# Kernel tuning notes

Hardware: AMD Instinct MI355X
Metric: run time of the kernel (lower is better)

## Reference

```python
import jax, jax.numpy as jnp
import numpy as np

CONTEXT_SIZE = 32
NDIM = 64
HEAD_SIZE = 64
BATCH = 16384


def setup_inputs() -> dict:
    key = jax.random.key(0)
    kx, kk, kq, kv = jax.random.split(key, 4)
    x = jax.random.normal(kx, (BATCH, CONTEXT_SIZE, NDIM), dtype=jnp.float32)
    # nn.Linear(ndim, head_size, bias=False): y = x @ W.T, W is [head_size, ndim].
    # We store transposed weights [ndim, head_size] so y = x @ W.
    scale = 1.0 / np.sqrt(NDIM)
    Wk = jax.random.normal(kk, (NDIM, HEAD_SIZE), dtype=jnp.float32) * scale
    Wq = jax.random.normal(kq, (NDIM, HEAD_SIZE), dtype=jnp.float32) * scale
    Wv = jax.random.normal(kv, (NDIM, HEAD_SIZE), dtype=jnp.float32) * scale
    return {"x": x, "Wk": Wk, "Wq": Wq, "Wv": Wv}


def reference(x, Wk, Wq, Wv):
    # x: [B, T, D] with T == CONTEXT_SIZE
    k = x @ Wk  # [B, T, H]
    q = x @ Wq  # [B, T, H]
    v = x @ Wv  # [B, T, H]
    # Faithful to source: p = q @ k^T / head_size**(-0.5) == q @ k^T * sqrt(head_size)
    p = jnp.einsum("bth,bsh->bts", q, k) * jnp.sqrt(jnp.float32(HEAD_SIZE))
    causal = jnp.tril(jnp.ones((CONTEXT_SIZE, CONTEXT_SIZE), dtype=bool))
    p = jnp.where(causal, p, -jnp.inf)
    p = jax.nn.softmax(p, axis=-1)
    # dropout is identity in eval mode
    return jnp.einsum("bts,bsh->bth", p, v)  # [B, T, H]
```

## Files before the change

kernel.cpp:

```cpp
#include <hip/hip_runtime.h>

typedef __attribute__((ext_vector_type(8))) short short8;
typedef __attribute__((ext_vector_type(4))) float f32x4;
typedef __attribute__((ext_vector_type(2))) unsigned int u32x2;

#define CTX 32
#define ND  64
#define NH  64
#define LOG2E_8 11.541560327111707f
#define NB_PER_WAVE 2

#define OFF_MH 0
#define OFF_ML 8192
#define OFF_WAVE 16384
#define PWSTR 80
#define PW_RTH 0
#define PW_RTL 2560
#define PW_VT  0
#define PW_P   4096
#define WAVE_BYTES 6144
#define LDS_BYTES (OFF_WAVE + 4 * WAVE_BYTES)

__device__ __forceinline__ unsigned short f2bf(float f) {
  unsigned int u = __builtin_bit_cast(unsigned int, f);
  u += 0x7FFFu + ((u >> 16) & 1u);
  return (unsigned short)(u >> 16);
}
__device__ __forceinline__ float bf2f(unsigned short b) {
  unsigned int u = ((unsigned int)b) << 16;
  return __builtin_bit_cast(float, u);
}
__device__ __forceinline__ unsigned int pk2(float a, float b) {
  return (unsigned int)f2bf(a) | ((unsigned int)f2bf(b) << 16);
}

#define MFMA(a, b, c) __builtin_amdgcn_mfma_f32_16x16x32_bf16((a), (b), (c), 0, 0, 0)

__global__ __launch_bounds__(256) void mk_m(
    const float* __restrict__ Wq, const float* __restrict__ Wk,
    const float* __restrict__ Wv,
    unsigned short* __restrict__ MtH, unsigned short* __restrict__ MtL,
    unsigned short* __restrict__ WvT)
{
  const int idx = blockIdx.x * 256 + threadIdx.x;
  const int dp = idx >> 6, d = idx & 63;
  const float* wq = Wq + d * 64;
  const float* wk = Wk + dp * 64;
  float acc = 0.f;
  #pragma unroll
  for (int h = 0; h < 64; ++h) acc = fmaf(wq[h], wk[h], acc);
  acc *= LOG2E_8;
  const unsigned short hi = f2bf(acc);
  MtH[idx] = hi;
  MtL[idx] = f2bf(acc - bf2f(hi));
  WvT[idx] = f2bf(Wv[d * 64 + dp]);
}

__device__ __forceinline__ void load_x(const float* __restrict__ xb,
                                       f32x4 (&xr)[2][2][2], int c, int g) {
  #pragma unroll
  for (int mt = 0; mt < 2; ++mt)
    #pragma unroll
    for (int kt = 0; kt < 2; ++kt) {
      const float* p = xb + (16 * mt + c) * ND + 32 * kt + 8 * g;
      xr[mt][kt][0] = *(const f32x4*)(p);
      xr[mt][kt][1] = *(const f32x4*)(p + 4);
    }
}

__device__ __forceinline__ void compute_batch(
    const f32x4 (&xr)[2][2][2], const short8 (&bvr)[4][2], char* lds, char* wl,
    float* __restrict__ ob, int c, int g)
{
  short8 xh[2][2], xl[2][2];
  #pragma unroll
  for (int mt = 0; mt < 2; ++mt) {
    #pragma unroll
    for (int kt = 0; kt < 2; ++kt) {
      short8 hi, lo;
      #pragma unroll
      for (int half = 0; half < 2; ++half) {
        #pragma unroll
        for (int j = 0; j < 4; ++j) {
          const float f = xr[mt][kt][half][j];
          const unsigned short h = f2bf(f);
          hi[4 * half + j] = (short)h;
          lo[4 * half + j] = (short)f2bf(f - bf2f(h));
        }
      }
      xh[mt][kt] = hi;
      xl[mt][kt] = lo;
    }
  }

  f32x4 pa[2][2] = {{{0.f,0.f,0.f,0.f},{0.f,0.f,0.f,0.f}},
                    {{0.f,0.f,0.f,0.f},{0.f,0.f,0.f,0.f}}};
  #pragma unroll
  for (int kt = 0; kt < 2; ++kt) {
    #pragma unroll
    for (int ntl = 0; ntl < 2; ++ntl) {
      const int nt = 2 * kt + ntl;
      f32x4 a0 = {0.f, 0.f, 0.f, 0.f};
      f32x4 a1 = {0.f, 0.f, 0.f, 0.f};
      #pragma unroll
      for (int kk = 0; kk < 2; ++kk) {
        const int row = 16 * nt + c;
        const int byte = row * 128 + ((64 * kk + 16 * g) ^ ((row & 7) << 4));
        const short8 bh = *(const short8*)(lds + OFF_MH + byte);
        const short8 bl = *(const short8*)(lds + OFF_ML + byte);
        a0 = MFMA(xh[0][kk], bh, a0);
        a0 = MFMA(xh[0][kk], bl, a0);
        a0 = MFMA(xl[0][kk], bh, a0);
        a1 = MFMA(xh[1][kk], bh, a1);
        a1 = MFMA(xh[1][kk], bl, a1);
        a1 = MFMA(xl[1][kk], bh, a1);
      }
      #pragma unroll
      for (int j = 0; j < 4; ++j) {
        const int col2 = 2 * (16 * ntl + c);
        const int off0 = (4 * g + j) * PWSTR + col2;
        const int off1 = (16 + 4 * g + j) * PWSTR + col2;
        const unsigned short h0 = f2bf(a0[j]);
        *(unsigned short*)(wl + PW_RTH + off0) = h0;
        *(unsigned short*)(wl + PW_RTL + off0) = f2bf(a0[j] - bf2f(h0));
        const unsigned short h1 = f2bf(a1[j]);
        *(unsigned short*)(wl + PW_RTH + off1) = h1;
        *(unsigned short*)(wl + PW_RTL + off1) = f2bf(a1[j] - bf2f(h1));
      }
    }
    short8 tH[2], tL[2];
    #pragma unroll
    for (int i = 0; i < 2; ++i) {
      const int off = (16 * i + c) * PWSTR + 16 * g;
      tH[i] = *(const short8*)(wl + PW_RTH + off);
      tL[i] = *(const short8*)(wl + PW_RTL + off);
    }
    #pragma unroll
    for (int mt = 0; mt < 2; ++mt) {
      #pragma unroll
      for (int nt2 = 0; nt2 < 2; ++nt2) {
        pa[mt][nt2] = MFMA(xh[mt][kt], tH[nt2], pa[mt][nt2]);
        pa[mt][nt2] = MFMA(xl[mt][kt], tH[nt2], pa[mt][nt2]);
        pa[mt][nt2] = MFMA(xh[mt][kt], tL[nt2], pa[mt][nt2]);
      }
    }
  }

  char* const pbuf = wl + PW_P;
  #pragma unroll
  for (int nt = 0; nt < 2; ++nt) {
    const int t = 16 * nt + c;
    float v[8];
    #pragma unroll
    for (int mt = 0; mt < 2; ++mt)
      #pragma unroll
      for (int j = 0; j < 4; ++j) {
        const int s = 16 * mt + 4 * g + j;
        v[4 * mt + j] = (s <= t) ? pa[mt][nt][j] : -__builtin_inff();
      }
    float m = fmaxf(fmaxf(fmaxf(v[0], v[1]), fmaxf(v[2], v[3])),
                    fmaxf(fmaxf(v[4], v[5]), fmaxf(v[6], v[7])));
    m = fmaxf(m, __shfl_xor(m, 16));
    m = fmaxf(m, __shfl_xor(m, 32));
    float e[8], ssum = 0.f;
    #pragma unroll
    for (int i = 0; i < 8; ++i) { e[i] = exp2f(v[i] - m); ssum += e[i]; }
    ssum += __shfl_xor(ssum, 16);
    ssum += __shfl_xor(ssum, 32);
    const float r = __builtin_amdgcn_rcpf(ssum);
    #pragma unroll
    for (int mt = 0; mt < 2; ++mt) {
      const u32x2 w2 = {pk2(e[4 * mt] * r, e[4 * mt + 1] * r),
                        pk2(e[4 * mt + 2] * r, e[4 * mt + 3] * r)};
      *(u32x2*)(pbuf + t * 64 + 32 * mt + 8 * g) = w2;
    }
  }

  #pragma unroll
  for (int nt = 0; nt < 4; ++nt) {
    f32x4 a0 = {0.f, 0.f, 0.f, 0.f};
    f32x4 a1 = {0.f, 0.f, 0.f, 0.f};
    #pragma unroll
    for (int kk = 0; kk < 2; ++kk) {
      a0 = MFMA(xh[0][kk], bvr[nt][kk], a0);
      a1 = MFMA(xh[1][kk], bvr[nt][kk], a1);
    }
    char* const vrow = wl + PW_VT + (16 * nt + c) * 64;
    const u32x2 w0 = {pk2(a0[0], a0[1]), pk2(a0[2], a0[3])};
    const u32x2 w1 = {pk2(a1[0], a1[1]), pk2(a1[2], a1[3])};
    *(u32x2*)(vrow + 8 * g)      = w0;
    *(u32x2*)(vrow + 32 + 8 * g) = w1;
  }

  const short8 ap0 = *(const short8*)(pbuf + c * 64 + 16 * g);
  const short8 ap1 = *(const short8*)(pbuf + (16 + c) * 64 + 16 * g);
  #pragma unroll
  for (int mh = 0; mh < 4; ++mh) {
    const short8 bv = *(const short8*)(wl + PW_VT + (16 * mh + c) * 64 + 16 * g);
    f32x4 o0 = {0.f, 0.f, 0.f, 0.f};
    f32x4 o1 = {0.f, 0.f, 0.f, 0.f};
    o0 = MFMA(bv, ap0, o0);
    o1 = MFMA(bv, ap1, o1);
    *(f32x4*)(ob + c * NH + 16 * mh + 4 * g)        = o0;
    *(f32x4*)(ob + (16 + c) * NH + 16 * mh + 4 * g) = o1;
  }
}

__global__ __launch_bounds__(256, 3) void head_fused(
    const float* __restrict__ x,
    const unsigned short* __restrict__ MtH, const unsigned short* __restrict__ MtL,
    const unsigned short* __restrict__ WvT,
    float* __restrict__ out, int wstride)
{
  __shared__ __align__(16) char lds[LDS_BYTES];
  const int tid = threadIdx.x;

  {
    const unsigned int* srcH = (const unsigned int*)MtH;
    const unsigned int* srcL = (const unsigned int*)MtL;
    #pragma unroll
    for (int i = 0; i < 8; ++i) {
      const int e = tid + 256 * i;
      const int row = e >> 5;
      const int byte = row * 128 + (((e & 31) * 4) ^ ((row & 7) << 4));
      *(unsigned int*)(lds + OFF_MH + byte) = srcH[e];
      *(unsigned int*)(lds + OFF_ML + byte) = srcL[e];
    }
  }
  __syncthreads();

  const int wid  = tid >> 6;
  const int lane = tid & 63;
  const int c = lane & 15;
  const int g = lane >> 4;
  char* const wl = lds + OFF_WAVE + wid * WAVE_BYTES;

  short8 bvr[4][2];
  #pragma unroll
  for (int nt = 0; nt < 4; ++nt)
    #pragma unroll
    for (int kk = 0; kk < 2; ++kk)
      bvr[nt][kk] = *(const short8*)(WvT + (16 * nt + c) * 64 + 32 * kk + 8 * g);

  const int w = blockIdx.x * 4 + wid;

  f32x4 xc[2][2][2];
  load_x(x + (long)w * (CTX * ND), xc, c, g);

  #pragma unroll
  for (int it = 0; it < NB_PER_WAVE; ++it) {
    const long b = (long)w + (long)it * wstride;
    f32x4 xn[2][2][2];
    if (it + 1 < NB_PER_WAVE)
      load_x(x + (b + wstride) * (CTX * ND), xn, c, g);
    compute_batch(xc, bvr, lds, wl, out + b * (CTX * NH), c, g);
    if (it + 1 < NB_PER_WAVE) {
      #pragma unroll
      for (int i = 0; i < 2; ++i)
        #pragma unroll
        for (int k = 0; k < 2; ++k)
          #pragma unroll
          for (int h = 0; h < 2; ++h) xc[i][k][h] = xn[i][k][h];
    }
  }
}

extern "C" void kernel_launch(void* const* d_in, const int* in_sizes, int n_in,
                              void* d_out, int out_size, void* d_ws, size_t ws_size,
                              hipStream_t stream) {
  const float* x  = (const float*)d_in[0];
  const float* Wk = (const float*)d_in[1];
  const float* Wq = (const float*)d_in[2];
  const float* Wv = (const float*)d_in[3];
  float* out = (float*)d_out;

  unsigned short* MtH = (unsigned short*)d_ws;
  unsigned short* MtL = MtH + 64 * 64;
  unsigned short* WvT = MtL + 64 * 64;

  mk_m<<<dim3(16), dim3(256), 0, stream>>>(Wq, Wk, Wv, MtH, MtL, WvT);

  const int batch = in_sizes[0] / (CTX * ND);
  const int wstride = batch / NB_PER_WAVE;
  head_fused<<<dim3(wstride / 4), dim3(256), 0, stream>>>(x, MtH, MtL, WvT, out, wstride);
}
```

Measured before the change: 72.69 us.

## Interleave two batches per wave to overlap independent MFMA chains

Each wave now processes two adjacent batches at once instead of two strided batches in sequence. The stages (QK fill, consume, softmax, V projection, PV) are interleaved between batch A and batch B so their independent MFMA and LDS work can hide each other's latency. Per-wave LDS scratch doubles, and the V buffer now uses a padded 80-byte row stride to cut bank conflicts. Launch bounds drop from 3 to 2 blocks per SM because register and LDS use grow, which lowers occupancy. Both x loads are now issued up front rather than prefetched during compute.

```diff
diff --git a/kernel.cpp b/kernel.cpp
--- a/kernel.cpp
+++ b/kernel.cpp
@@ -8,7 +8,6 @@
 #define ND  64
 #define NH  64
 #define LOG2E_8 11.541560327111707f
-#define NB_PER_WAVE 2
 
 #define OFF_MH 0
 #define OFF_ML 8192
@@ -17,9 +16,10 @@
 #define PW_RTH 0
 #define PW_RTL 2560
 #define PW_VT  0
-#define PW_P   4096
-#define WAVE_BYTES 6144
-#define LDS_BYTES (OFF_WAVE + 4 * WAVE_BYTES)
+#define PW_P   5120
+#define WAVE_BYTES 7168
+#define NREG 8
+#define LDS_BYTES (OFF_WAVE + NREG * WAVE_BYTES)
 
 __device__ __forceinline__ unsigned short f2bf(float f) {
   unsigned int u = __builtin_bit_cast(unsigned int, f);
@@ -56,6 +56,13 @@
   WvT[idx] = f2bf(Wv[d * 64 + dp]);
 }
 
+struct Batch {
+  short8 xh[2][2], xl[2][2];
+  f32x4  pa[2][2];
+  char*  wl;
+  float* ob;
+};
+
 __device__ __forceinline__ void load_x(const float* __restrict__ xb,
                                        f32x4 (&xr)[2][2][2], int c, int g) {
   #pragma unroll
@@ -68,18 +75,14 @@
     }
 }
 
-__device__ __forceinline__ void compute_batch(
-    const f32x4 (&xr)[2][2][2], const short8 (&bvr)[4][2], char* lds, char* wl,
-    float* __restrict__ ob, int c, int g)
-{
-  short8 xh[2][2], xl[2][2];
-  #pragma unroll
-  for (int mt = 0; mt < 2; ++mt) {
+__device__ __forceinline__ void split_x(Batch& s, const f32x4 (&xr)[2][2][2]) {
+  #pragma unroll
+  for (int mt = 0; mt < 2; ++mt)
     #pragma unroll
     for (int kt = 0; kt < 2; ++kt) {
       short8 hi, lo;
       #pragma unroll
-      for (int half = 0; half < 2; ++half) {
+      for (int half = 0; half < 2; ++half)
         #pragma unroll
         for (int j = 0; j < 4; ++j) {
           const float f = xr[mt][kt][half][j];
@@ -87,66 +90,67 @@
           hi[4 * half + j] = (short)h;
           lo[4 * half + j] = (short)f2bf(f - bf2f(h));
         }
-      }
-      xh[mt][kt] = hi;
-      xl[mt][kt] = lo;
-    }
-  }
-
-  f32x4 pa[2][2] = {{{0.f,0.f,0.f,0.f},{0.f,0.f,0.f,0.f}},
-                    {{0.f,0.f,0.f,0.f},{0.f,0.f,0.f,0.f}}};
-  #pragma unroll
-  for (int kt = 0; kt < 2; ++kt) {
-    #pragma unroll
-    for (int ntl = 0; ntl < 2; ++ntl) {
-      const int nt = 2 * kt + ntl;
-      f32x4 a0 = {0.f, 0.f, 0.f, 0.f};
-      f32x4 a1 = {0.f, 0.f, 0.f, 0.f};
-      #pragma unroll
-      for (int kk = 0; kk < 2; ++kk) {
-        const int row = 16 * nt + c;
-        const int byte = row * 128 + ((64 * kk + 16 * g) ^ ((row & 7) << 4));
-        const short8 bh = *(const short8*)(lds + OFF_MH + byte);
-        const short8 bl = *(const short8*)(lds + OFF_ML + byte);
-        a0 = MFMA(xh[0][kk], bh, a0);
-        a0 = MFMA(xh[0][kk], bl, a0);
-        a0 = MFMA(xl[0][kk], bh, a0);
-        a1 = MFMA(xh[1][kk], bh, a1);
-        a1 = MFMA(xh[1][kk], bl, a1);
-        a1 = MFMA(xl[1][kk], bh, a1);
-      }
-      #pragma unroll
-      for (int j = 0; j < 4; ++j) {
-        const int col2 = 2 * (16 * ntl + c);
-        const int off0 = (4 * g + j) * PWSTR + col2;
-        const int off1 = (16 + 4 * g + j) * PWSTR + col2;
-        const unsigned short h0 = f2bf(a0[j]);
-        *(unsigned short*)(wl + PW_RTH + off0) = h0;
-        *(unsigned short*)(wl + PW_RTL + off0) = f2bf(a0[j] - bf2f(h0));
-        const unsigned short h1 = f2bf(a1[j]);
-        *(unsigned short*)(wl + PW_RTH + off1) = h1;
-        *(unsigned short*)(wl + PW_RTL + off1) = f2bf(a1[j] - bf2f(h1));
-      }
-    }
-    short8 tH[2], tL[2];
-    #pragma unroll
-    for (int i = 0; i < 2; ++i) {
-      const int off = (16 * i + c) * PWSTR + 16 * g;
-      tH[i] = *(const short8*)(wl + PW_RTH + off);
-      tL[i] = *(const short8*)(wl + PW_RTL + off);
-    }
-    #pragma unroll
-    for (int mt = 0; mt < 2; ++mt) {
-      #pragma unroll
-      for (int nt2 = 0; nt2 < 2; ++nt2) {
-        pa[mt][nt2] = MFMA(xh[mt][kt], tH[nt2], pa[mt][nt2]);
-        pa[mt][nt2] = MFMA(xl[mt][kt], tH[nt2], pa[mt][nt2]);
-        pa[mt][nt2] = MFMA(xh[mt][kt], tL[nt2], pa[mt][nt2]);
-      }
-    }
-  }
-
-  char* const pbuf = wl + PW_P;
+      s.xh[mt][kt] = hi;
+      s.xl[mt][kt] = lo;
+    }
+  #pragma unroll
+  for (int i = 0; i < 2; ++i)
+    #pragma unroll
+    for (int j = 0; j < 2; ++j) s.pa[i][j] = f32x4{0.f, 0.f, 0.f, 0.f};
+}
+
+__device__ __forceinline__ void qk_fill(Batch& s, const char* lds,
+                                        int kt, int ntl, int c, int g) {
+  const int nt = 2 * kt + ntl;
+  f32x4 a0 = {0.f, 0.f, 0.f, 0.f};
+  f32x4 a1 = {0.f, 0.f, 0.f, 0.f};
+  #pragma unroll
+  for (int kk = 0; kk < 2; ++kk) {
+    const int row = 16 * nt + c;
+    const int byte = row * 128 + ((64 * kk + 16 * g) ^ ((row & 7) << 4));
+    const short8 bh = *(const short8*)(lds + OFF_MH + byte);
+    const short8 bl = *(const short8*)(lds + OFF_ML + byte);
+    a0 = MFMA(s.xh[0][kk], bh, a0);
+    a0 = MFMA(s.xh[0][kk], bl, a0);
+    a0 = MFMA(s.xl[0][kk], bh, a0);
+    a1 = MFMA(s.xh[1][kk], bh, a1);
+    a1 = MFMA(s.xh[1][kk], bl, a1);
+    a1 = MFMA(s.xl[1][kk], bh, a1);
+  }
+  #pragma unroll
+  for (int j = 0; j < 4; ++j) {
+    const int col2 = 2 * (16 * ntl + c);
+    const int off0 = (4 * g + j) * PWSTR + col2;
+    const int off1 = (16 + 4 * g + j) * PWSTR + col2;
+    const unsigned short h0 = f2bf(a0[j]);
+    *(unsigned short*)(s.wl + PW_RTH + off0) = h0;
+    *(unsigned short*)(s.wl + PW_RTL + off0) = f2bf(a0[j] - bf2f(h0));
+    const unsigned short h1 = f2bf(a1[j]);
+    *(unsigned short*)(s.wl + PW_RTH + off1) = h1;
+    *(unsigned short*)(s.wl + PW_RTL + off1) = f2bf(a1[j] - bf2f(h1));
+  }
+}
+
+__device__ __forceinline__ void qk_consume(Batch& s, int kt, int c, int g) {
+  short8 tH[2], tL[2];
+  #pragma unroll
+  for (int i = 0; i < 2; ++i) {
+    const int off = (16 * i + c) * PWSTR + 16 * g;
+    tH[i] = *(const short8*)(s.wl + PW_RTH + off);
+    tL[i] = *(const short8*)(s.wl + PW_RTL + off);
+  }
+  #pragma unroll
+  for (int mt = 0; mt < 2; ++mt)
+    #pragma unroll
+    for (int nt2 = 0; nt2 < 2; ++nt2) {
+      s.pa[mt][nt2] = MFMA(s.xh[mt][kt], tH[nt2], s.pa[mt][nt2]);
+      s.pa[mt][nt2] = MFMA(s.xl[mt][kt], tH[nt2], s.pa[mt][nt2]);
+      s.pa[mt][nt2] = MFMA(s.xh[mt][kt], tL[nt2], s.pa[mt][nt2]);
+    }
+}
+
+__device__ __forceinline__ void softmax_store(Batch& s, int c, int g) {
+  char* const pbuf = s.wl + PW_P;
   #pragma unroll
   for (int nt = 0; nt < 2; ++nt) {
     const int t = 16 * nt + c;
@@ -155,8 +159,8 @@
     for (int mt = 0; mt < 2; ++mt)
       #pragma unroll
       for (int j = 0; j < 4; ++j) {
-        const int s = 16 * mt + 4 * g + j;
-        v[4 * mt + j] = (s <= t) ? pa[mt][nt][j] : -__builtin_inff();
+        const int sidx = 16 * mt + 4 * g + j;
+        v[4 * mt + j] = (sidx <= t) ? s.pa[mt][nt][j] : -__builtin_inff();
       }
     float m = fmaxf(fmaxf(fmaxf(v[0], v[1]), fmaxf(v[2], v[3])),
                     fmaxf(fmaxf(v[4], v[5]), fmaxf(v[6], v[7])));
@@ -175,42 +179,48 @@
       *(u32x2*)(pbuf + t * 64 + 32 * mt + 8 * g) = w2;
     }
   }
-
+}
+
+__device__ __forceinline__ void vproj(Batch& s, const short8 (&bvr)[4][2],
+                                      int c, int g) {
   #pragma unroll
   for (int nt = 0; nt < 4; ++nt) {
     f32x4 a0 = {0.f, 0.f, 0.f, 0.f};
     f32x4 a1 = {0.f, 0.f, 0.f, 0.f};
     #pragma unroll
     for (int kk = 0; kk < 2; ++kk) {
-      a0 = MFMA(xh[0][kk], bvr[nt][kk], a0);
-      a1 = MFMA(xh[1][kk], bvr[nt][kk], a1);
-    }
-    char* const vrow = wl + PW_VT + (16 * nt + c) * 64;
+      a0 = MFMA(s.xh[0][kk], bvr[nt][kk], a0);
+      a1 = MFMA(s.xh[1][kk], bvr[nt][kk], a1);
+    }
+    char* const vrow = s.wl + PW_VT + (16 * nt + c) * PWSTR;
     const u32x2 w0 = {pk2(a0[0], a0[1]), pk2(a0[2], a0[3])};
     const u32x2 w1 = {pk2(a1[0], a1[1]), pk2(a1[2], a1[3])};
     *(u32x2*)(vrow + 8 * g)      = w0;
     *(u32x2*)(vrow + 32 + 8 * g) = w1;
   }
-
+}
+
+__device__ __forceinline__ void pv_store(Batch& s, int c, int g) {
+  char* const pbuf = s.wl + PW_P;
   const short8 ap0 = *(const short8*)(pbuf + c * 64 + 16 * g);
   const short8 ap1 = *(const short8*)(pbuf + (16 + c) * 64 + 16 * g);
   #pragma unroll
   for (int mh = 0; mh < 4; ++mh) {
-    const short8 bv = *(const short8*)(wl + PW_VT + (16 * mh + c) * 64 + 16 * g);
+    const short8 bv = *(const short8*)(s.wl + PW_VT + (16 * mh + c) * PWSTR + 16 * g);
     f32x4 o0 = {0.f, 0.f, 0.f, 0.f};
     f32x4 o1 = {0.f, 0.f, 0.f, 0.f};
     o0 = MFMA(bv, ap0, o0);
     o1 = MFMA(bv, ap1, o1);
-    *(f32x4*)(ob + c * NH + 16 * mh + 4 * g)        = o0;
-    *(f32x4*)(ob + (16 + c) * NH + 16 * mh + 4 * g) = o1;
-  }
-}
-
-__global__ __launch_bounds__(256, 3) void head_fused(
+    *(f32x4*)(s.ob + c * NH + 16 * mh + 4 * g)        = o0;
+    *(f32x4*)(s.ob + (16 + c) * NH + 16 * mh + 4 * g) = o1;
+  }
+}
+
+__global__ __launch_bounds__(256, 2) void head_fused(
     const float* __restrict__ x,
     const unsigned short* __restrict__ MtH, const unsigned short* __restrict__ MtL,
     const unsigned short* __restrict__ WvT,
-    float* __restrict__ out, int wstride)
+    float* __restrict__ out)
 {
   __shared__ __align__(16) char lds[LDS_BYTES];
   const int tid = threadIdx.x;
@@ -233,7 +243,6 @@
   const int lane = tid & 63;
   const int c = lane & 15;
   const int g = lane >> 4;
-  char* const wl = lds + OFF_WAVE + wid * WAVE_BYTES;
 
   short8 bvr[4][2];
   #pragma unroll
@@ -243,26 +252,36 @@
       bvr[nt][kk] = *(const short8*)(WvT + (16 * nt + c) * 64 + 32 * kk + 8 * g);
 
   const int w = blockIdx.x * 4 + wid;
-
-  f32x4 xc[2][2][2];
-  load_x(x + (long)w * (CTX * ND), xc, c, g);
-
-  #pragma unroll
-  for (int it = 0; it < NB_PER_WAVE; ++it) {
-    const long b = (long)w + (long)it * wstride;
-    f32x4 xn[2][2][2];
-    if (it + 1 < NB_PER_WAVE)
-      load_x(x + (b + wstride) * (CTX * ND), xn, c, g);
-    compute_batch(xc, bvr, lds, wl, out + b * (CTX * NH), c, g);
-    if (it + 1 < NB_PER_WAVE) {
-      #pragma unroll
-      for (int i = 0; i < 2; ++i)
-        #pragma unroll
-        for (int k = 0; k < 2; ++k)
-          #pragma unroll
-          for (int h = 0; h < 2; ++h) xc[i][k][h] = xn[i][k][h];
-    }
-  }
+  const long bA = 2L * w, bB = 2L * w + 1;
+
+  Batch A, B;
+  A.wl = lds + OFF_WAVE + (wid * 2 + 0) * WAVE_BYTES;
+  B.wl = lds + OFF_WAVE + (wid * 2 + 1) * WAVE_BYTES;
+  A.ob = out + bA * (CTX * NH);
+  B.ob = out + bB * (CTX * NH);
+
+  f32x4 xrA[2][2][2], xrB[2][2][2];
+  load_x(x + bA * (CTX * ND), xrA, c, g);
+  load_x(x + bB * (CTX * ND), xrB, c, g);
+
+  split_x(A, xrA);
+  split_x(B, xrB);
+
+  #pragma unroll
+  for (int kt = 0; kt < 2; ++kt) {
+    qk_fill(A, lds, kt, 0, c, g);
+    qk_fill(B, lds, kt, 0, c, g);
+    qk_fill(A, lds, kt, 1, c, g);
+    qk_fill(B, lds, kt, 1, c, g);
+    qk_consume(A, kt, c, g);
+    qk_consume(B, kt, c, g);
+  }
+  softmax_store(A, c, g);
+  softmax_store(B, c, g);
+  vproj(A, bvr, c, g);
+  vproj(B, bvr, c, g);
+  pv_store(A, c, g);
+  pv_store(B, c, g);
 }
 
 extern "C" void kernel_launch(void* const* d_in, const int* in_sizes, int n_in,
@@ -281,6 +300,6 @@
   mk_m<<<dim3(16), dim3(256), 0, stream>>>(Wq, Wk, Wv, MtH, MtL, WvT);
 
   const int batch = in_sizes[0] / (CTX * ND);
-  const int wstride = batch / NB_PER_WAVE;
-  head_fused<<<dim3(wstride / 4), dim3(256), 0, stream>>>(x, MtH, MtL, WvT, out, wstride);
-}
+  const int nwg = batch / 8;
+  head_fused<<<dim3(nwg), dim3(256), 0, stream>>>(x, MtH, MtL, WvT, out);
+}
```

Result: faster. 64.26 us (-11.6%).
